# Optimization experiments

Measured on AMD Instinct MI355X. Metric: run time of the kernel, lower is better.

Reference implementation:

```python
import jax, jax.numpy as jnp
import numpy as np

VOCAB, DEC_VOCAB, E, H, T = 256, 128, 1024, 2048, 1025

def setup_inputs() -> dict:
    key = jax.random.key(0)
    ks = jax.random.split(key, 8)
    return {
        "x": jax.random.randint(ks[0], (T,), 0, VOCAB),
        "len_words": T - 1,  # scalar python int
        "enc_emb": jax.random.normal(ks[1], (VOCAB, E), jnp.float32) * 0.02,
        "enc_w_ih": jax.random.normal(ks[2], (3 * H, E), jnp.float32) * 0.02,
        "enc_w_hh": jax.random.normal(ks[3], (3 * H, H), jnp.float32) * 0.02,
        "enc_b_ih": jax.random.normal(ks[4], (3 * H,), jnp.float32) * 0.02,
        "enc_b_hh": jax.random.normal(ks[5], (3 * H,), jnp.float32) * 0.02,
        "dec_emb": jax.random.normal(ks[6], (DEC_VOCAB, E), jnp.float32) * 0.02,
    }

def _gru_scan(xs, w_ih, w_hh, b_ih, b_hh):
    # xs: [T, 1, E]; returns final hidden [1, H]
    h_dim = w_hh.shape[1]
    def cell(h, xt):
        rzn_ih = xt @ w_ih.T + b_ih            # [1, 3H]
        rzn_hh = h @ w_hh.T + b_hh             # [1, 3H]
        rz = jax.nn.sigmoid(rzn_ih[:, :2 * h_dim] + rzn_hh[:, :2 * h_dim])
        r, z = rz[:, :h_dim], rz[:, h_dim:]
        n = jnp.tanh(rzn_ih[:, 2 * h_dim:] + r * rzn_hh[:, 2 * h_dim:])
        h = (1.0 - z) * n + z * h
        return h, None
    h0 = jnp.zeros((1, h_dim), jnp.float32)
    h_last, _ = jax.lax.scan(cell, h0, xs)
    return h_last

def reference(x, len_words, enc_emb, enc_w_ih, enc_w_hh, enc_b_ih, enc_b_hh, dec_emb):
    steps = int(len_words) + 1
    emb = enc_emb[x[:steps]]                   # [steps, E]
    xs = emb[:, None, :]                       # [steps, 1, E] (batch 1)
    h = _gru_scan(xs, enc_w_ih, enc_w_hh, enc_b_ih, enc_b_hh)  # [1, H]
    dec = dec_emb[2][None, None, :]            # [1, 1, E]
    return dec, h
```

## Files before the change

kernel.cpp:

```cpp
#include <hip/hip_runtime.h>
#include <hip/hip_bf16.h>
#include <math.h>

#define E_DIM 1024
#define H_DIM 2048
#define H3 6144
#define VOCAB 256
#define NCOMP 256
#define TPW 512

typedef unsigned long long u64;

__global__ __launch_bounds__(256) void ih_table_kernel(
    const float* __restrict__ emb, const float* __restrict__ w_ih,
    const float* __restrict__ b_ih, float* __restrict__ table)
{
    __shared__ float As[32][65];
    __shared__ float Bs[32][65];
    const int v0 = blockIdx.y * 64;
    const int j0 = blockIdx.x * 64;
    const int t  = threadIdx.x;
    const int tx = t % 16, ty = t / 16;
    const int lr0 = t / 8;
    const int lc  = (t % 8) * 4;
    float acc[4][4] = {};

    for (int k0 = 0; k0 < E_DIM; k0 += 32) {
        __syncthreads();
#pragma unroll
        for (int p = 0; p < 2; ++p) {
            int r = lr0 + p * 32;
            float4 a = *(const float4*)(emb  + (size_t)(v0 + r) * E_DIM + k0 + lc);
            As[lc+0][r] = a.x; As[lc+1][r] = a.y; As[lc+2][r] = a.z; As[lc+3][r] = a.w;
            float4 b = *(const float4*)(w_ih + (size_t)(j0 + r) * E_DIM + k0 + lc);
            Bs[lc+0][r] = b.x; Bs[lc+1][r] = b.y; Bs[lc+2][r] = b.z; Bs[lc+3][r] = b.w;
        }
        __syncthreads();
#pragma unroll 8
        for (int kk = 0; kk < 32; ++kk) {
            float a4[4], b4[4];
#pragma unroll
            for (int i = 0; i < 4; ++i) a4[i] = As[kk][ty * 4 + i];
#pragma unroll
            for (int i = 0; i < 4; ++i) b4[i] = Bs[kk][tx * 4 + i];
#pragma unroll
            for (int i = 0; i < 4; ++i)
#pragma unroll
                for (int j = 0; j < 4; ++j) acc[i][j] += a4[i] * b4[j];
        }
    }
    const int j = j0 + tx * 4;
    float4 bias = *(const float4*)(b_ih + j);
#pragma unroll
    for (int i = 0; i < 4; ++i) {
        int v = v0 + ty * 4 + i;
        float4 o;
        o.x = acc[i][0] + bias.x; o.y = acc[i][1] + bias.y;
        o.z = acc[i][2] + bias.z; o.w = acc[i][3] + bias.w;
        *(float4*)(table + (size_t)v * H3 + j) = o;
    }
}

__global__ __launch_bounds__(TPW, 2) void gru_persistent(
    const int* __restrict__ x, const int* __restrict__ lenp,
    const float* __restrict__ w_hh, const float* __restrict__ b_hh,
    const float* __restrict__ table,
    u64* hbuf0, u64* hbuf1)
{
    __shared__ float hsh[2][H_DIM];
    const int cw   = blockIdx.x;
    const int tid  = threadIdx.x;
    const int base = cw * 8;
    const int uu   = tid >> 6;
    const int l    = tid & 63;
    const int S    = lenp[0] + 1;

    float4 wv[3][8];
#pragma unroll
    for (int g = 0; g < 3; ++g) {
        const float4* wr =
            (const float4*)(w_hh + (size_t)(g * H_DIM + base + uu) * H_DIM);
#pragma unroll
        for (int i = 0; i < 8; ++i) wv[g][i] = wr[i * 64 + l];
    }
#pragma unroll
    for (int g = 0; g < 3; ++g)
#pragma unroll
        for (int i = 0; i < 8; ++i)
            asm volatile("" : "+v"(wv[g][i].x), "+v"(wv[g][i].y),
                              "+v"(wv[g][i].z), "+v"(wv[g][i].w));

    float bhr = 0.f, bhz = 0.f, bhn = 0.f;
    if (l == 0) {
        bhr = b_hh[base + uu];
        bhz = b_hh[H_DIM + base + uu];
        bhn = b_hh[2 * H_DIM + base + uu];
    }

    u64* bufs[2] = {hbuf0, hbuf1};

    for (int s = 0; s < S; ++s) {
        const u64* src = bufs[s & 1];
        u64*       dst = bufs[(s + 1) & 1];
        float*     hs  = hsh[s & 1];

        float ihr = 0.f, ihz = 0.f, ihn = 0.f;
        if (l == 0) {
            const float* trow = table + (size_t)x[s] * H3;
            ihr = trow[base + uu];
            ihz = trow[H_DIM + base + uu];
            ihn = trow[2 * H_DIM + base + uu];
        }

        {
            const unsigned want = (unsigned)s;
            const u64* ps = src + 4 * tid;
            float* hd = hs + 4 * tid;
            bool ok[4] = {false, false, false, false};
            int rem = 4;
            while (rem) {
#pragma unroll
                for (int j = 0; j < 4; ++j) {
                    if (!ok[j]) {
                        u64 v = __hip_atomic_load(ps + j, __ATOMIC_RELAXED,
                                                  __HIP_MEMORY_SCOPE_AGENT);
                        if ((unsigned)(v >> 32) == want) {
                            ok[j] = true; --rem;
                            hd[j] = __uint_as_float((unsigned)v);
                        }
                    }
                }
                if (rem) __builtin_amdgcn_s_sleep(1);
            }
        }
        __syncthreads();

        const float4* h4 = (const float4*)hs;
        float4 ar = make_float4(0.f, 0.f, 0.f, 0.f);
        float4 az = make_float4(0.f, 0.f, 0.f, 0.f);
        float4 an = make_float4(0.f, 0.f, 0.f, 0.f);
#pragma unroll
        for (int i = 0; i < 8; ++i) {
            float4 hv = h4[i * 64 + l];
            ar.x += wv[0][i].x * hv.x; ar.y += wv[0][i].y * hv.y;
            ar.z += wv[0][i].z * hv.z; ar.w += wv[0][i].w * hv.w;
            az.x += wv[1][i].x * hv.x; az.y += wv[1][i].y * hv.y;
            az.z += wv[1][i].z * hv.z; az.w += wv[1][i].w * hv.w;
            an.x += wv[2][i].x * hv.x; an.y += wv[2][i].y * hv.y;
            an.z += wv[2][i].z * hv.z; an.w += wv[2][i].w * hv.w;
        }
        float pr = (ar.x + ar.y) + (ar.z + ar.w);
        float pz = (az.x + az.y) + (az.z + az.w);
        float pn = (an.x + an.y) + (an.z + an.w);
#pragma unroll
        for (int d = 1; d < 64; d <<= 1) {
            pr += __shfl_xor(pr, d);
            pz += __shfl_xor(pz, d);
            pn += __shfl_xor(pn, d);
        }

        if (l == 0) {
            float hprev = hs[base + uu];
            float hr = pr + bhr;
            float hz = pz + bhz;
            float hn = pn + bhn;
            float r_ = 1.f / (1.f + __expf(-(ihr + hr)));
            float z_ = 1.f / (1.f + __expf(-(ihz + hz)));
            float xn = ihn + r_ * hn;
            float axn = fabsf(xn), te = __expf(2.f * axn);
            float n_ = copysignf(1.f - 2.f / (te + 1.f), xn);
            float hnew = (1.f - z_) * n_ + z_ * hprev;
            u64 pack = ((u64)(unsigned)(s + 1) << 32) |
                       (u64)__float_as_uint(hnew);
            __hip_atomic_store(dst + base + uu, pack, __ATOMIC_RELAXED,
                               __HIP_MEMORY_SCOPE_AGENT);
        }
    }
}

__global__ void epilogue_kernel(const int* __restrict__ lenp,
                                const float* __restrict__ dec_emb,
                                const u64* __restrict__ hbuf0,
                                const u64* __restrict__ hbuf1,
                                float* __restrict__ out)
{
    int i = blockIdx.x * blockDim.x + threadIdx.x;
    int S = lenp[0] + 1;
    const u64* hb = (S & 1) ? hbuf1 : hbuf0;
    if (i < E_DIM) out[i] = dec_emb[2 * E_DIM + i];
    else if (i < E_DIM + H_DIM)
        out[i] = __uint_as_float((unsigned)hb[i - E_DIM]);
}

extern "C" void kernel_launch(void* const* d_in, const int* in_sizes, int n_in,
                              void* d_out, int out_size, void* d_ws, size_t ws_size,
                              hipStream_t stream) {
    const int*   x       = (const int*)d_in[0];
    const int*   lenp    = (const int*)d_in[1];
    const float* emb     = (const float*)d_in[2];
    const float* w_ih    = (const float*)d_in[3];
    const float* w_hh    = (const float*)d_in[4];
    const float* b_ih    = (const float*)d_in[5];
    const float* b_hh    = (const float*)d_in[6];
    const float* dec_emb = (const float*)d_in[7];
    float* out = (float*)d_out;

    char* ws = (char*)d_ws;
    float* table = (float*)ws;
    u64*   hbuf0 = (u64*)(ws + (size_t)VOCAB * H3 * 4);
    u64*   hbuf1 = hbuf0 + H_DIM;

    hipMemsetAsync(hbuf0, 0, (size_t)2 * H_DIM * sizeof(u64), stream);

    dim3 gA(H3 / 64, VOCAB / 64);
    ih_table_kernel<<<gA, 256, 0, stream>>>(emb, w_ih, b_ih, table);

    gru_persistent<<<dim3(NCOMP), dim3(TPW), 0, stream>>>(
        x, lenp, w_hh, b_hh, table, hbuf0, hbuf1);

    epilogue_kernel<<<12, 256, 0, stream>>>(lenp, dec_emb, hbuf0, hbuf1, out);
}
```

Before: 2.904 ms.

## Replace per-element tagged hidden-state polling with per-block release flags

Before, each hidden value was stored as a 64-bit word carrying a step tag, and every thread polled four such words until all tags matched. Now each block publishes its 8 plain float outputs, then one thread does a release store of a per-block step counter. Consumers spin on that flag and then read the data with a cache-bypassing vector load. This cuts polling traffic and halves the data size, but adds an extra barrier per step and a serial flag-then-data round trip, and it drops the second shared-memory buffer.

New measurement: 7.363 ms. 154% more time.

```diff
diff --git a/kernel.cpp b/kernel.cpp
--- a/kernel.cpp
+++ b/kernel.cpp
@@ -10,6 +10,8 @@
 #define TPW 512
 
 typedef unsigned long long u64;
+typedef unsigned int u32;
+typedef float f32x4 __attribute__((ext_vector_type(4)));
 
 __global__ __launch_bounds__(256) void ih_table_kernel(
     const float* __restrict__ emb, const float* __restrict__ w_ih,
@@ -65,9 +67,9 @@
     const int* __restrict__ x, const int* __restrict__ lenp,
     const float* __restrict__ w_hh, const float* __restrict__ b_hh,
     const float* __restrict__ table,
-    u64* hbuf0, u64* hbuf1)
+    float* d0, float* d1, u32* flags)
 {
-    __shared__ float hsh[2][H_DIM];
+    __shared__ float hsh[H_DIM];
     const int cw   = blockIdx.x;
     const int tid  = threadIdx.x;
     const int base = cw * 8;
@@ -97,12 +99,14 @@
         bhn = b_hh[2 * H_DIM + base + uu];
     }
 
-    u64* bufs[2] = {hbuf0, hbuf1};
+    float* bufs[2] = {d0, d1};
+    const u64* flags64 = (const u64*)flags;
+    const int  fidx = tid >> 2;
+    const int  fsh  = ((tid >> 1) & 1) * 32;
 
     for (int s = 0; s < S; ++s) {
-        const u64* src = bufs[s & 1];
-        u64*       dst = bufs[(s + 1) & 1];
-        float*     hs  = hsh[s & 1];
+        const float* src = bufs[s & 1];
+        u32*         dst = (u32*)bufs[(s + 1) & 1];
 
         float ihr = 0.f, ihz = 0.f, ihn = 0.f;
         if (l == 0) {
@@ -114,28 +118,26 @@
 
         {
             const unsigned want = (unsigned)s;
-            const u64* ps = src + 4 * tid;
-            float* hd = hs + 4 * tid;
-            bool ok[4] = {false, false, false, false};
-            int rem = 4;
-            while (rem) {
-#pragma unroll
-                for (int j = 0; j < 4; ++j) {
-                    if (!ok[j]) {
-                        u64 v = __hip_atomic_load(ps + j, __ATOMIC_RELAXED,
-                                                  __HIP_MEMORY_SCOPE_AGENT);
-                        if ((unsigned)(v >> 32) == want) {
-                            ok[j] = true; --rem;
-                            hd[j] = __uint_as_float((unsigned)v);
-                        }
-                    }
-                }
-                if (rem) __builtin_amdgcn_s_sleep(1);
+            const u64* fp = flags64 + fidx;
+            for (;;) {
+                u64 fv = __hip_atomic_load(fp, __ATOMIC_RELAXED,
+                                           __HIP_MEMORY_SCOPE_AGENT);
+                if ((u32)(fv >> fsh) >= want) break;
+                __builtin_amdgcn_s_sleep(1);
             }
         }
-        __syncthreads();
-
-        const float4* h4 = (const float4*)hs;
+
+        {
+            const float* dp = src + 4 * tid;
+            f32x4 dv;
+            asm volatile("global_load_dwordx4 %0, %1, off sc0 sc1\n\t"
+                         "s_waitcnt vmcnt(0)"
+                         : "=v"(dv) : "v"(dp) : "memory");
+            *(f32x4*)(hsh + 4 * tid) = dv;
+        }
+        __syncthreads();
+
+        const float4* h4 = (const float4*)hsh;
         float4 ar = make_float4(0.f, 0.f, 0.f, 0.f);
         float4 az = make_float4(0.f, 0.f, 0.f, 0.f);
         float4 an = make_float4(0.f, 0.f, 0.f, 0.f);
@@ -160,7 +162,7 @@
         }
 
         if (l == 0) {
-            float hprev = hs[base + uu];
+            float hprev = hsh[base + uu];
             float hr = pr + bhr;
             float hz = pz + bhz;
             float hn = pn + bhn;
@@ -170,26 +172,28 @@
             float axn = fabsf(xn), te = __expf(2.f * axn);
             float n_ = copysignf(1.f - 2.f / (te + 1.f), xn);
             float hnew = (1.f - z_) * n_ + z_ * hprev;
-            u64 pack = ((u64)(unsigned)(s + 1) << 32) |
-                       (u64)__float_as_uint(hnew);
-            __hip_atomic_store(dst + base + uu, pack, __ATOMIC_RELAXED,
-                               __HIP_MEMORY_SCOPE_AGENT);
-        }
+            __hip_atomic_store(dst + base + uu, __float_as_uint(hnew),
+                               __ATOMIC_RELAXED, __HIP_MEMORY_SCOPE_AGENT);
+        }
+        __syncthreads();
+        if (tid == 0)
+            __hip_atomic_store(flags + cw, (u32)(s + 1),
+                               __ATOMIC_RELEASE, __HIP_MEMORY_SCOPE_AGENT);
     }
 }
 
 __global__ void epilogue_kernel(const int* __restrict__ lenp,
                                 const float* __restrict__ dec_emb,
-                                const u64* __restrict__ hbuf0,
-                                const u64* __restrict__ hbuf1,
+                                const float* __restrict__ d0,
+                                const float* __restrict__ d1,
                                 float* __restrict__ out)
 {
     int i = blockIdx.x * blockDim.x + threadIdx.x;
     int S = lenp[0] + 1;
-    const u64* hb = (S & 1) ? hbuf1 : hbuf0;
+    const float* hb = (S & 1) ? d1 : d0;
     if (i < E_DIM) out[i] = dec_emb[2 * E_DIM + i];
     else if (i < E_DIM + H_DIM)
-        out[i] = __uint_as_float((unsigned)hb[i - E_DIM]);
+        out[i] = hb[i - E_DIM];
 }
 
 extern "C" void kernel_launch(void* const* d_in, const int* in_sizes, int n_in,
@@ -200,23 +204,25 @@
     const float* emb     = (const float*)d_in[2];
     const float* w_ih    = (const float*)d_in[3];
     const float* w_hh    = (const float*)d_in[4];
+    const float* b_hh    = (const float*)d_in[6];
     const float* b_ih    = (const float*)d_in[5];
-    const float* b_hh    = (const float*)d_in[6];
     const float* dec_emb = (const float*)d_in[7];
     float* out = (float*)d_out;
 
     char* ws = (char*)d_ws;
     float* table = (float*)ws;
-    u64*   hbuf0 = (u64*)(ws + (size_t)VOCAB * H3 * 4);
-    u64*   hbuf1 = hbuf0 + H_DIM;
-
-    hipMemsetAsync(hbuf0, 0, (size_t)2 * H_DIM * sizeof(u64), stream);
+    float* d0    = (float*)(ws + (size_t)VOCAB * H3 * 4);
+    float* d1    = d0 + H_DIM;
+    u32*   flags = (u32*)(d1 + H_DIM);
+
+    hipMemsetAsync(d0, 0, (size_t)2 * H_DIM * sizeof(float) + NCOMP * sizeof(u32),
+                   stream);
 
     dim3 gA(H3 / 64, VOCAB / 64);
     ih_table_kernel<<<gA, 256, 0, stream>>>(emb, w_ih, b_ih, table);
 
     gru_persistent<<<dim3(NCOMP), dim3(TPW), 0, stream>>>(
-        x, lenp, w_hh, b_hh, table, hbuf0, hbuf1);
-
-    epilogue_kernel<<<12, 256, 0, stream>>>(lenp, dec_emb, hbuf0, hbuf1, out);
-}
+        x, lenp, w_hh, b_hh, table, d0, d1, flags);
+
+    epilogue_kernel<<<12, 256, 0, stream>>>(lenp, dec_emb, d0, d1, out);
+}
```
